# Kernel tuning notes

Hardware: AMD Instinct MI355X
Metric: run time of the kernel (lower is better)

The kernel has to match this reference:

```python
import jax, jax.numpy as jnp
import numpy as np

# ---- static config (from init_kwargs) ----
CANVAS = (4, 32, 32)        # (C1, C2, C3) latent video canvas
TILE = (4, 8, 8)            # (T1, T2, T3) tile dims
KERNEL = (1, 3, 3)          # sliding kernel in tile units
ROPE_DIMS = (16, 56, 56)    # per-axis RoPE dims, sums to head_dim
THETA = 256.0
HEADS = 16
HEAD_DIM = 128
HIDDEN = HEADS * HEAD_DIM
B = 1
L = CANVAS[0] * CANVAS[1] * CANVAS[2]
EPS = 1e-6
SCALE = HEAD_DIM ** -0.5
D = tuple(CANVAS[i] // TILE[i] for i in range(3))   # tile grid (D1,D2,D3)
N_TILES = D[0] * D[1] * D[2]
T_TOK = TILE[0] * TILE[1] * TILE[2]


def _rope_tables():
    # 3D meshgrid positions, per-axis 1D rotary tables concatenated on feature dim
    grids = np.meshgrid(*[np.arange(c, dtype=np.float32) for c in CANVAS], indexing='ij')
    cos_l, sin_l = [], []
    for i in range(3):
        dim = ROPE_DIMS[i]
        freqs = 1.0 / (THETA ** (np.arange(0, dim, 2, dtype=np.float32) / dim))
        ang = grids[i].reshape(-1)[:, None] * freqs[None, :]          # [L, dim/2]
        cos_l.append(np.repeat(np.cos(ang), 2, axis=1))               # [L, dim]
        sin_l.append(np.repeat(np.sin(ang), 2, axis=1))
    return jnp.asarray(np.concatenate(cos_l, 1)), jnp.asarray(np.concatenate(sin_l, 1))


def _window_indices():
    # For each query tile (d1,d2,d3): attends to a clamped kernel window of kv tiles
    d1, d2, d3 = np.meshgrid(*[np.arange(d) for d in D], indexing='ij')
    idx = []
    for i, dg in enumerate((d1, d2, d3)):
        k = KERNEL[i]
        s = np.clip(dg - k // 2, 0, D[i] - k)                         # window start, [D1,D2,D3]
        shape = [1, 1, 1]
        shape[i] = k
        idx.append(s[..., None, None, None] + np.arange(k).reshape(shape))
    flat = (idx[0] * D[1] + idx[1]) * D[2] + idx[2]                   # [D1,D2,D3,k1,k2,k3]
    kt = KERNEL[0] * KERNEL[1] * KERNEL[2]
    return jnp.asarray(flat.reshape(N_TILES, kt))


def _tile(x):
    # [B,H,L,E] -> [B,H,N_tiles,T_tok,E] with (D1,T1,D2,T2,D3,T3) -> (D1,D2,D3,T1,T2,T3)
    b, h, _, e = x.shape
    x = x.reshape(b, h, D[0], TILE[0], D[1], TILE[1], D[2], TILE[2], e)
    x = x.transpose(0, 1, 2, 4, 6, 3, 5, 7, 8)
    return x.reshape(b, h, N_TILES, T_TOK, e)


def _untile(x):
    # inverse of _tile: [B,H,N_tiles,T_tok,E] -> [B,H,L,E]
    b, h, _, _, e = x.shape
    x = x.reshape(b, h, D[0], D[1], D[2], TILE[0], TILE[1], TILE[2], e)
    x = x.transpose(0, 1, 2, 5, 3, 6, 4, 7, 8)
    return x.reshape(b, h, L, e)


def _rms(x, g):
    return x * jax.lax.rsqrt(jnp.mean(x * x, axis=-1, keepdims=True) + EPS) * g


def _rope(x, cos, sin):
    # x: [B,L,H,E], cos/sin: [L,E]; rotate-half in interleaved pairs
    xr = x.reshape(*x.shape[:-1], HEAD_DIM // 2, 2)
    rot = jnp.stack([-xr[..., 1], xr[..., 0]], axis=-1).reshape(x.shape)
    return x * cos[None, :, None, :] + rot * sin[None, :, None, :]


def _forward(hidden_states, Wq, bq, Wk, bk, Wv, bv, Wo, bo, gq, gk):
    cos, sin = _rope_tables()
    q = hidden_states @ Wq + bq
    k = hidden_states @ Wk + bk
    v = hidden_states @ Wv + bv
    q = q.reshape(B, L, HEADS, HEAD_DIM)
    k = k.reshape(B, L, HEADS, HEAD_DIM)
    v = v.reshape(B, L, HEADS, HEAD_DIM)
    q = _rope(_rms(q, gq), cos, sin)
    k = _rope(_rms(k, gk), cos, sin)
    q = q.transpose(0, 2, 1, 3)  # [B,H,L,E]
    k = k.transpose(0, 2, 1, 3)
    v = v.transpose(0, 2, 1, 3)
    qt = _tile(q)                # [B,H,N,T,E]
    kt = _tile(k)
    vt = _tile(v)
    win = _window_indices()      # [N, Kt]
    kt_w = kt[:, :, win].reshape(B, HEADS, N_TILES, -1, HEAD_DIM)  # [B,H,N,Kt*T,E]
    vt_w = vt[:, :, win].reshape(B, HEADS, N_TILES, -1, HEAD_DIM)
    s = jnp.einsum('bhnqe,bhnke->bhnqk', qt, kt_w) * SCALE
    p = jax.nn.softmax(s, axis=-1)
    o = jnp.einsum('bhnqk,bhnke->bhnqe', p, vt_w)
    o = _untile(o).transpose(0, 2, 1, 3).reshape(B, L, HIDDEN)
    return o @ Wo + bo


def setup_inputs() -> dict:
    key = jax.random.key(0)
    ks = jax.random.split(key, 6)
    w = 0.02
    return {
        'hidden_states': jax.random.normal(ks[0], (B, L, HIDDEN), jnp.float32),
        'Wq': jax.random.normal(ks[1], (HIDDEN, HIDDEN), jnp.float32) * w,
        'bq': jnp.zeros((HIDDEN,), jnp.float32),
        'Wk': jax.random.normal(ks[2], (HIDDEN, HIDDEN), jnp.float32) * w,
        'bk': jnp.zeros((HIDDEN,), jnp.float32),
        'Wv': jax.random.normal(ks[3], (HIDDEN, HIDDEN), jnp.float32) * w,
        'bv': jnp.zeros((HIDDEN,), jnp.float32),
        'Wo': jax.random.normal(ks[4], (HIDDEN, HIDDEN), jnp.float32) * w,
        'bo': jnp.zeros((HIDDEN,), jnp.float32),
        'gq': jnp.ones((HEAD_DIM,), jnp.float32),
        'gk': jnp.ones((HEAD_DIM,), jnp.float32),
    }


def reference(hidden_states, Wq, bq, Wk, bk, Wv, bv, Wo, bo, gq, gk):
    return _forward(hidden_states, Wq, bq, Wk, bk, Wv, bv, Wo, bo, gq, gk)
```

## Files before the change

### kernel.cpp

```cpp
#include <hip/hip_runtime.h>
#include <math.h>

typedef __attribute__((ext_vector_type(8))) short bf16x8;
typedef __attribute__((ext_vector_type(4))) float f32x4;
typedef unsigned short u16;
typedef unsigned int u32;

#define N_TOK 4096
#define HID   2048
#define N_HEAD 16
#define HDIM  128
#define QK_SCALE 0.08838834764831845f
#define LOG2E_   1.4426950408889634f

__device__ __forceinline__ u16 f2bf(float x) {
  union { float f; u32 u; } v; v.f = x;
  u32 r = v.u + 0x7fffu + ((v.u >> 16) & 1u);
  return (u16)(r >> 16);
}

__device__ __forceinline__ u32 cvtpk(float lo, float hi) {
  u32 r;
  asm("v_cvt_pk_bf16_f32 %0, %1, %2" : "=v"(r) : "v"(lo), "v"(hi));
  return r;
}

__device__ __forceinline__ void async16(const void* g, void* l) {
  __builtin_amdgcn_global_load_lds(
      (const __attribute__((address_space(1))) void*)g,
      (__attribute__((address_space(3))) void*)l, 16, 0, 0);
}

#define MFMA(a, b, c) __builtin_amdgcn_mfma_f32_16x16x32_bf16((a), (b), (c), 0, 0, 0)

__global__ void k_rope(float* __restrict__ cosT, float* __restrict__ sinT) {
  int l = blockIdx.x;
  int p = threadIdx.x;
  int c1 = l >> 10, c2 = (l >> 5) & 31, c3 = l & 31;
  int pos, j; float dim;
  if (p < 8)       { pos = c1; j = p;      dim = 16.f; }
  else if (p < 36) { pos = c2; j = p - 8;  dim = 56.f; }
  else             { pos = c3; j = p - 36; dim = 56.f; }
  float freq = exp2f(-8.0f * (2.0f * (float)j) / dim);
  float ang = (float)pos * freq;
  float s, c;
  sincosf(ang, &s, &c);
  cosT[l * 64 + p] = c;
  sinT[l * 64 + p] = s;
}

__global__ __launch_bounds__(256) void k_cvt_x(const float* __restrict__ X, u16* __restrict__ Xb) {
  int i = blockIdx.x * 256 + threadIdx.x;
  float4 v = ((const float4*)X)[i];
  ushort4 o;
  o.x = f2bf(v.x); o.y = f2bf(v.y); o.z = f2bf(v.z); o.w = f2bf(v.w);
  ((ushort4*)Xb)[i] = o;
}

__global__ __launch_bounds__(256) void k_tw(const float* __restrict__ Wq, const float* __restrict__ Wk,
                                            const float* __restrict__ Wv, const float* __restrict__ Wo,
                                            u16* __restrict__ WT) {
  int z = blockIdx.z;
  const float* W = (z == 0) ? Wq : (z == 1) ? Wk : (z == 2) ? Wv : Wo;
  u16* dst = WT + (size_t)z * 2048 * 2048;
  __shared__ __align__(16) float T[64][69];
  int n0 = blockIdx.x * 64, k0 = blockIdx.y * 64;
  int tid = threadIdx.x;
  int r = tid >> 4, c4 = tid & 15;
#pragma unroll
  for (int i = 0; i < 4; ++i) {
    int row = r + i * 16;
    float4 v = *(const float4*)(W + (size_t)(k0 + row) * 2048 + n0 + c4 * 4);
    T[row][c4 * 4 + 0] = v.x; T[row][c4 * 4 + 1] = v.y;
    T[row][c4 * 4 + 2] = v.z; T[row][c4 * 4 + 3] = v.w;
  }
  __syncthreads();
#pragma unroll
  for (int i = 0; i < 4; ++i) {
    int row = r + i * 16;
    ushort4 o;
    o.x = f2bf(T[c4 * 4 + 0][row]);
    o.y = f2bf(T[c4 * 4 + 1][row]);
    o.z = f2bf(T[c4 * 4 + 2][row]);
    o.w = f2bf(T[c4 * 4 + 3][row]);
    *(ushort4*)(dst + (size_t)(n0 + row) * 2048 + k0 + c4 * 4) = o;
  }
}


#define VM8 asm volatile("s_waitcnt vmcnt(8)" ::: "memory");
#define VM6 asm volatile("s_waitcnt vmcnt(6)" ::: "memory");
#define VMNONE

#define STAGEU(SB, SAB, SH, ST) do {                                            \
    int st_ = (ST) < Tk ? (ST) : Tk - 1;                                        \
    const char* src_ = ((SAB) ? Bp : Ap) + (size_t)((SH) * 128) * Kb + (size_t)st_ * 128; \
    char* dstl_ = &Lds[SB][SAB][SH][0];                                         \
    _Pragma("unroll")                                                           \
    for (int i_ = 0; i_ < 2; ++i_) {                                            \
      int flat_ = tid + 512 * i_;                                               \
      int row_ = flat_ >> 3, sb_ = flat_ & 7;                                   \
      async16(src_ + (size_t)row_ * Kb + ((sb_ ^ (row_ & 7)) << 4), dstl_ + flat_ * 16); \
    }                                                                           \
  } while (0)

#define PHASE(BUF, MH, NH, READA, VMOP, SB, SAB, SH, ST) do {                   \
    VMOP                                                                        \
    __builtin_amdgcn_s_barrier();                                               \
    asm volatile("" ::: "memory");                                              \
    bf16x8 bb[2][2];                                                            \
    const char* Lm = &Lds[BUF][0][MH][0];                                       \
    const char* Ln = &Lds[BUF][1][NH][0];                                       \
    if (READA) {                                                                \
      _Pragma("unroll")                                                         \
      for (int kk = 0; kk < 2; ++kk)                                            \
        _Pragma("unroll")                                                       \
        for (int mf = 0; mf < 4; ++mf) {                                        \
          int row = wmIdx * 64 + mf * 16 + cl;                                  \
          af[kk][mf] = *(const bf16x8*)(Lm + row * 128 + (((kk * 4 + g) ^ (row & 7)) << 4)); \
        }                                                                       \
    }                                                                           \
    _Pragma("unroll")                                                           \
    for (int kk = 0; kk < 2; ++kk)                                              \
      _Pragma("unroll")                                                         \
      for (int nf = 0; nf < 2; ++nf) {                                          \
        int row = wnIdx * 32 + nf * 16 + cl;                                    \
        bb[kk][nf] = *(const bf16x8*)(Ln + row * 128 + (((kk * 4 + g) ^ (row & 7)) << 4)); \
      }                                                                         \
    STAGEU(SB, SAB, SH, ST);                                                    \
    __builtin_amdgcn_s_setprio(1);                                              \
    _Pragma("unroll")                                                           \
    for (int kk = 0; kk < 2; ++kk)                                              \
      _Pragma("unroll")                                                         \
      for (int mf = 0; mf < 4; ++mf)                                            \
        _Pragma("unroll")                                                       \
        for (int nf = 0; nf < 2; ++nf)                                          \
          acc[(MH) * 4 + mf][(NH) * 2 + nf] =                                   \
              MFMA(af[kk][mf], bb[kk][nf], acc[(MH) * 4 + mf][(NH) * 2 + nf]);  \
    __builtin_amdgcn_s_setprio(0);                                              \
  } while (0)

__global__ __launch_bounds__(512, 2) void k_gemm8(const u16* __restrict__ A, const u16* __restrict__ Bt,
                                                  const float* __restrict__ b0, const float* __restrict__ b1,
                                                  const float* __restrict__ b2, float* __restrict__ C,
                                                  int gn, int K, int ldc) {
  __shared__ __align__(16) char Lds[2][2][2][16384];
  int tid = threadIdx.x;
  int lane = tid & 63, wid = tid >> 6;
  int g = lane >> 4, cl = lane & 15;
  int wmIdx = wid >> 2, wnIdx = wid & 3;
  int nwg = gridDim.x;
  int wg = (int)blockIdx.x;
  int cpx = nwg >> 3;
  wg = (wg & 7) * cpx + (wg >> 3);
  int bm = wg / gn, bn = wg % gn;
  size_t Kb = (size_t)K * 2;
  const char* Ap = (const char*)A + (size_t)bm * 256 * Kb;
  const char* Bp = (const char*)Bt + (size_t)bn * 256 * Kb;
  int Tk = K >> 6;

  f32x4 acc[8][4] = {};
  bf16x8 af[2][4];

  STAGEU(0, 0, 0, 0);
  STAGEU(0, 1, 0, 0);
  STAGEU(0, 0, 1, 0);
  STAGEU(0, 1, 1, 0);
  STAGEU(1, 0, 0, 1);
  STAGEU(1, 1, 0, 1);

  int nIter = Tk >> 1;
  for (int it = 0; it < nIter; ++it) {
    int t = 2 * it;
    PHASE(0, 0, 0, 1, VM8,    1, 0, 1, t + 1);
    PHASE(0, 0, 1, 0, VM6,    1, 1, 1, t + 1);
    PHASE(0, 1, 0, 1, VMNONE, 0, 0, 0, t + 2);
    PHASE(0, 1, 1, 0, VMNONE, 0, 1, 0, t + 2);
    PHASE(1, 0, 0, 1, VM8,    0, 0, 1, t + 2);
    PHASE(1, 0, 1, 0, VM6,    0, 1, 1, t + 2);
    PHASE(1, 1, 0, 1, VMNONE, 1, 0, 0, t + 3);
    PHASE(1, 1, 1, 0, VMNONE, 1, 1, 0, t + 3);
  }

#pragma unroll
  for (int mfp = 0; mfp < 8; ++mfp) {
    int rowBase = (mfp < 4 ? wmIdx * 64 + mfp * 16 : 128 + wmIdx * 64 + (mfp - 4) * 16) + g * 4;
    int rowG = bm * 256 + rowBase;
#pragma unroll
    for (int nfp = 0; nfp < 4; ++nfp) {
      int colLoc = (nfp < 2 ? wnIdx * 32 + nfp * 16 : 128 + wnIdx * 32 + (nfp - 2) * 16) + cl;
      int col = bn * 256 + colLoc;
      int z = col >> 11;
      const float* bp = (z == 0) ? b0 : (z == 1) ? b1 : b2;
      float bv = bp[col & 2047];
#pragma unroll
      for (int rr = 0; rr < 4; ++rr)
        C[(size_t)(rowG + rr) * ldc + col] = acc[mfp][nfp][rr] + bv;
    }
  }
}

__global__ __launch_bounds__(256) void k_prep_qk(const float* __restrict__ src, int stride,
                                                 const float* __restrict__ gg,
                                                 const float* __restrict__ cosT, const float* __restrict__ sinT,
                                                 u16* __restrict__ dst, int isk) {
  int job = blockIdx.x * 4 + (threadIdx.x >> 6);
  int lane = threadIdx.x & 63;
  int tok = job & 4095, h = job >> 12;
  const float* row = src + (size_t)tok * stride + h * 128;
  float2 x = *(const float2*)(row + lane * 2);
  float ss = x.x * x.x + x.y * x.y;
#pragma unroll
  for (int m = 1; m < 64; m <<= 1) ss += __shfl_xor(ss, m, 64);
  float rms = rsqrtf(ss * (1.0f / 128.0f) + 1e-6f);
  float x0 = x.x * rms * gg[lane * 2];
  float x1 = x.y * rms * gg[lane * 2 + 1];
  float c = cosT[tok * 64 + lane], s = sinT[tok * 64 + lane];
  float y0 = x0 * c - x1 * s;
  float y1 = x1 * c + x0 * s;
  if (!isk) { y0 *= QK_SCALE * LOG2E_; y1 *= QK_SCALE * LOG2E_; }
  u32 pk = cvtpk(y0, y1);
  int c1 = tok >> 10, c2 = (tok >> 5) & 31, c3 = tok & 31;
  int n = (c2 >> 3) * 4 + (c3 >> 3);
  int t = c1 * 64 + (c2 & 7) * 8 + (c3 & 7);
  size_t rowidx = (size_t)(h * 16 + n) * 256 + t;
  if (!isk) {
    ((u32*)dst)[rowidx * 64 + lane] = pk;
  } else {
    char* base = (char*)dst + rowidx * 256;
    *(u32*)(base + ((((lane >> 2) ^ (t & 7)) << 4) + (lane & 3) * 4)) = pk;
  }
}

__global__ __launch_bounds__(256) void k_prep_v(const float* __restrict__ src, int stride,
                                                u16* __restrict__ Vt) {
  __shared__ __align__(16) u16 T[128][72];
  int tid = threadIdx.x;
  int h = blockIdx.x >> 6, n = (blockIdx.x >> 2) & 15, ch = blockIdx.x & 3;
  int d2 = n >> 2, d3 = n & 3;
  int tc = tid >> 2, cq = tid & 3;
  int tok = (ch * 32 + d2 * 8 + (tc >> 3)) * 32 + d3 * 8 + (tc & 7);
  const float* sp = src + (size_t)tok * stride + h * 128;
#pragma unroll
  for (int i = 0; i < 8; ++i) {
    int d0 = cq * 4 + i * 16;
    float4 v = *(const float4*)(sp + d0);
    T[d0 + 0][tc] = f2bf(v.x); T[d0 + 1][tc] = f2bf(v.y);
    T[d0 + 2][tc] = f2bf(v.z); T[d0 + 3][tc] = f2bf(v.w);
  }
  __syncthreads();
  int d = tid >> 1, half = tid & 1;
  char* dstb = (char*)Vt + ((size_t)((h * 16 + n) * 4 + ch) * 128 + d) * 128;
#pragma unroll
  for (int b = 0; b < 4; ++b) {
    int blk = half * 4 + b;
    uint4 val = *(const uint4*)&T[d][blk * 8];
    *(uint4*)(dstb + ((blk ^ (d & 7)) << 4)) = val;
  }
}

__global__ __launch_bounds__(512) void k_attn(const u16* __restrict__ Qt, const u16* __restrict__ Kt,
                                              const u16* __restrict__ Vt, u16* __restrict__ AO) {
  __shared__ __align__(16) char Kl[2][16384];
  __shared__ __align__(16) char Vl[2][16384];
  __shared__ __align__(16) char Pl[8][4096];
  int tid = threadIdx.x;
  int lane = tid & 63, wid = tid >> 6;
  int g = lane >> 4, cl = lane & 15;
  int bid = (int)blockIdx.x;
  int xcd = bid & 7, i = bid >> 3;
  int h = xcd * 2 + (i >> 4);
  int n = i & 15;
  int d2 = n >> 2, d3 = n & 3;
  int s2 = d2 - 1; s2 = s2 < 0 ? 0 : (s2 > 1 ? 1 : s2);
  int s3 = d3 - 1; s3 = s3 < 0 ? 0 : (s3 > 1 ? 1 : s3);
  int q0 = wid * 32;

  bf16x8 qf[2][4];
  const char* Qb = (const char*)Qt + (size_t)(h * 16 + n) * 256 * 256;
#pragma unroll
  for (int nq = 0; nq < 2; ++nq)
#pragma unroll
    for (int kf = 0; kf < 4; ++kf)
      qf[nq][kf] = *(const bf16x8*)(Qb + (q0 + nq * 16 + cl) * 256 + kf * 64 + g * 16);

  f32x4 o[2][8] = {};
  float L0 = 0.f, L1 = 0.f;

  auto stage = [&](int buf, int c) {
    int kvi = c >> 2, cc = c & 3;
    int i2 = kvi / 3, i3 = kvi - i2 * 3;
    int kvt = (s2 + i2) * 4 + (s3 + i3);
    const char* Kb = (const char*)Kt + ((size_t)((h * 16 + kvt) * 256 + cc * 64)) * 256;
    const char* Vb = (const char*)Vt + ((size_t)((h * 16 + kvt) * 4 + cc)) * 16384;
#pragma unroll
    for (int i_ = 0; i_ < 2; ++i_) {
      int flat = tid + 512 * i_;
      async16(Kb + flat * 16, &Kl[buf][0] + flat * 16);
      async16(Vb + flat * 16, &Vl[buf][0] + flat * 16);
    }
  };

  stage(0, 0);
  __syncthreads();

  char* Pw = &Pl[wid][0];
  for (int c = 0; c < 36; ++c) {
    int cur = c & 1;
    if (c + 1 < 36) stage(cur ^ 1, c + 1);
    const char* Kc = &Kl[cur][0];
    f32x4 st[4][2] = {};
    __builtin_amdgcn_s_setprio(1);
#pragma unroll
    for (int ks = 0; ks < 4; ++ks) {
      bf16x8 af[4];
#pragma unroll
      for (int mk = 0; mk < 4; ++mk) {
        int row = mk * 16 + cl;
        af[mk] = *(const bf16x8*)(Kc + row * 256 + (((ks * 4 + g) ^ (row & 7)) << 4));
      }
#pragma unroll
      for (int mk = 0; mk < 4; ++mk) {
        st[mk][0] = MFMA(af[mk], qf[0][ks], st[mk][0]);
        st[mk][1] = MFMA(af[mk], qf[1][ks], st[mk][1]);
      }
    }
    __builtin_amdgcn_s_setprio(0);
#pragma unroll
    for (int mk = 0; mk < 4; ++mk)
#pragma unroll
      for (int r = 0; r < 4; ++r) {
        float p0 = exp2f(st[mk][0][r]);
        float p1 = exp2f(st[mk][1][r]);
        st[mk][0][r] = p0; L0 += p0;
        st[mk][1][r] = p1; L1 += p1;
      }
#pragma unroll
    for (int nq = 0; nq < 2; ++nq) {
      int q = nq * 16 + cl;
#pragma unroll
      for (int mk = 0; mk < 4; ++mk)
#pragma unroll
        for (int rp = 0; rp < 2; ++rp) {
          u32 pk = cvtpk(st[mk][nq][rp * 2], st[mk][nq][rp * 2 + 1]);
          int kv = mk * 16 + g * 4 + rp * 2;
          *(u32*)(Pw + q * 128 + (((kv >> 3) ^ (q & 7)) << 4) + (kv & 7) * 2) = pk;
        }
    }
    const char* Vc = &Vl[cur][0];
    __builtin_amdgcn_s_setprio(1);
#pragma unroll
    for (int ks = 0; ks < 2; ++ks) {
      bf16x8 pf0, pf1, vf[8];
      {
        int q = cl;
        pf0 = *(const bf16x8*)(Pw + q * 128 + (((ks * 4 + g) ^ (q & 7)) << 4));
        q = 16 + cl;
        pf1 = *(const bf16x8*)(Pw + q * 128 + (((ks * 4 + g) ^ (q & 7)) << 4));
      }
#pragma unroll
      for (int nd = 0; nd < 8; ++nd) {
        int d = nd * 16 + cl;
        vf[nd] = *(const bf16x8*)(Vc + d * 128 + (((ks * 4 + g) ^ (d & 7)) << 4));
      }
#pragma unroll
      for (int nd = 0; nd < 8; ++nd) {
        o[0][nd] = MFMA(pf0, vf[nd], o[0][nd]);
        o[1][nd] = MFMA(pf1, vf[nd], o[1][nd]);
      }
    }
    __builtin_amdgcn_s_setprio(0);
    __syncthreads();
  }
  L0 += __shfl_xor(L0, 16, 64); L0 += __shfl_xor(L0, 32, 64);
  L1 += __shfl_xor(L1, 16, 64); L1 += __shfl_xor(L1, 32, 64);
  float lr0[4], lr1[4];
#pragma unroll
  for (int r = 0; r < 4; ++r) {
    lr0[r] = 1.0f / __shfl(L0, g * 4 + r, 64);
    lr1[r] = 1.0f / __shfl(L1, g * 4 + r, 64);
  }
#pragma unroll
  for (int mo = 0; mo < 2; ++mo)
#pragma unroll
    for (int r = 0; r < 4; ++r) {
      int t = q0 + mo * 16 + g * 4 + r;
      int t1 = t >> 6, t2 = (t >> 3) & 7, t3 = t & 7;
      int tok = (t1 * 32 + d2 * 8 + t2) * 32 + d3 * 8 + t3;
      u16* orow = AO + (size_t)tok * HID + h * HDIM;
      float lr = (mo == 0) ? lr0[r] : lr1[r];
#pragma unroll
      for (int nd = 0; nd < 8; ++nd)
        orow[nd * 16 + cl] = f2bf(o[mo][nd][r] * lr);
    }
}

extern "C" void kernel_launch(void* const* d_in, const int* in_sizes, int n_in,
                              void* d_out, int out_size, void* d_ws, size_t ws_size,
                              hipStream_t stream) {
  const float* X  = (const float*)d_in[0];
  const float* Wq = (const float*)d_in[1];
  const float* bq = (const float*)d_in[2];
  const float* Wk = (const float*)d_in[3];
  const float* bk = (const float*)d_in[4];
  const float* Wv = (const float*)d_in[5];
  const float* bv = (const float*)d_in[6];
  const float* Wo = (const float*)d_in[7];
  const float* bo = (const float*)d_in[8];
  const float* gq = (const float*)d_in[9];
  const float* gk = (const float*)d_in[10];

  char* ws = (char*)d_ws;
  size_t off = 0;
  auto alloc = [&](size_t bytes) { void* p = ws + off; off = (off + bytes + 255) & ~(size_t)255; return p; };

  u16*   Xb  = (u16*)alloc((size_t)N_TOK * HID * 2);
  u16*   WT  = (u16*)alloc((size_t)4 * 2048 * 2048 * 2);
  float* COS = (float*)alloc((size_t)N_TOK * 64 * 4);
  float* SIN = (float*)alloc((size_t)N_TOK * 64 * 4);
  u16*   Qt  = (u16*)alloc((size_t)N_TOK * HID * 2);
  u16*   Kt  = (u16*)alloc((size_t)N_TOK * HID * 2);
  u16*   Vt  = (u16*)alloc((size_t)N_TOK * HID * 2);
  u16*   AO  = (u16*)alloc((size_t)N_TOK * HID * 2);
  size_t fixed = off;
  size_t needF = fixed + (size_t)N_TOK * 6144 * 4 + 256;
  bool fused = (ws_size >= needF);
  float* PF = (float*)alloc(fused ? (size_t)N_TOK * 6144 * 4 : (size_t)N_TOK * 2048 * 4);
  float* OUT = (float*)d_out;

  k_rope<<<N_TOK, 64, 0, stream>>>(COS, SIN);
  k_cvt_x<<<(N_TOK * HID / 4) / 256, 256, 0, stream>>>(X, Xb);
  k_tw<<<dim3(32, 32, 4), 256, 0, stream>>>(Wq, Wk, Wv, Wo, WT);

  if (fused) {
    k_gemm8<<<16 * 24, 512, 0, stream>>>(Xb, WT, bq, bk, bv, PF, 24, 2048, 6144);
    k_prep_qk<<<16384, 256, 0, stream>>>(PF + 0,    6144, gq, COS, SIN, Qt, 0);
    k_prep_qk<<<16384, 256, 0, stream>>>(PF + 2048, 6144, gk, COS, SIN, Kt, 1);
    k_prep_v <<<1024,  256, 0, stream>>>(PF + 4096, 6144, Vt);
  } else {
    k_gemm8<<<16 * 8, 512, 0, stream>>>(Xb, WT + (size_t)0 * 2048 * 2048, bq, bq, bq, PF, 8, 2048, 2048);
    k_prep_qk<<<16384, 256, 0, stream>>>(PF, 2048, gq, COS, SIN, Qt, 0);
    k_gemm8<<<16 * 8, 512, 0, stream>>>(Xb, WT + (size_t)1 * 2048 * 2048, bk, bk, bk, PF, 8, 2048, 2048);
    k_prep_qk<<<16384, 256, 0, stream>>>(PF, 2048, gk, COS, SIN, Kt, 1);
    k_gemm8<<<16 * 8, 512, 0, stream>>>(Xb, WT + (size_t)2 * 2048 * 2048, bv, bv, bv, PF, 8, 2048, 2048);
    k_prep_v<<<1024, 256, 0, stream>>>(PF, 2048, Vt);
  }

  k_attn<<<256, 512, 0, stream>>>(Qt, Kt, Vt, AO);

  k_gemm8<<<16 * 8, 512, 0, stream>>>(AO, WT + (size_t)3 * 2048 * 2048, bo, bo, bo, OUT, 8, 2048, 2048);
}
```

Baseline: 460.8 us.

## Restructure GEMM main loop into reordered quadrant pipeline with XCD-aware tile mapping

Rewrites the 256x256 bf16 GEMM main loop from eight fixed phases per two k-steps into four MFMA quadrants per k-step. B fragments are kept in two register sets and reused across quadrants in the order (0,0),(0,1),(1,1),(1,0), and LDS reads, async global stages and barriers are interleaved around them. It also replaces the generic XCD swizzle with a fixed mapping that groups M and N tiles per XCD for L2 reuse. The extra barriers, and the mapping's assumption about the grid shape (bm spanning 16 row tiles, gn divisible by 4), add sync cost and could give wrong tile coverage for other shapes.

```diff
diff --git a/kernel.cpp b/kernel.cpp
--- a/kernel.cpp
+++ b/kernel.cpp
@@ -88,9 +88,7 @@
 }
 
 
-#define VM8 asm volatile("s_waitcnt vmcnt(8)" ::: "memory");
 #define VM6 asm volatile("s_waitcnt vmcnt(6)" ::: "memory");
-#define VMNONE
 
 #define STAGEU(SB, SAB, SH, ST) do {                                            \
     int st_ = (ST) < Tk ? (ST) : Tk - 1;                                        \
@@ -104,30 +102,31 @@
     }                                                                           \
   } while (0)
 
-#define PHASE(BUF, MH, NH, READA, VMOP, SB, SAB, SH, ST) do {                   \
-    VMOP                                                                        \
-    __builtin_amdgcn_s_barrier();                                               \
-    asm volatile("" ::: "memory");                                              \
-    bf16x8 bb[2][2];                                                            \
-    const char* Lm = &Lds[BUF][0][MH][0];                                       \
-    const char* Ln = &Lds[BUF][1][NH][0];                                       \
-    if (READA) {                                                                \
+#define RD_A(HALF) do {                                                         \
+    const char* Lm_ = &Lds[buf][0][HALF][0];                                    \
+    _Pragma("unroll")                                                           \
+    for (int kk = 0; kk < 2; ++kk)                                              \
       _Pragma("unroll")                                                         \
-      for (int kk = 0; kk < 2; ++kk)                                            \
-        _Pragma("unroll")                                                       \
-        for (int mf = 0; mf < 4; ++mf) {                                        \
-          int row = wmIdx * 64 + mf * 16 + cl;                                  \
-          af[kk][mf] = *(const bf16x8*)(Lm + row * 128 + (((kk * 4 + g) ^ (row & 7)) << 4)); \
-        }                                                                       \
-    }                                                                           \
+      for (int mf = 0; mf < 4; ++mf) {                                          \
+        int row = wmIdx * 64 + mf * 16 + cl;                                    \
+        af[kk][mf] = *(const bf16x8*)(Lm_ + row * 128 + (((kk * 4 + g) ^ (row & 7)) << 4)); \
+      }                                                                         \
+  } while (0)
+
+#define RD_B(DST, HALF) do {                                                    \
+    const char* Ln_ = &Lds[buf][1][HALF][0];                                    \
     _Pragma("unroll")                                                           \
     for (int kk = 0; kk < 2; ++kk)                                              \
       _Pragma("unroll")                                                         \
       for (int nf = 0; nf < 2; ++nf) {                                          \
         int row = wnIdx * 32 + nf * 16 + cl;                                    \
-        bb[kk][nf] = *(const bf16x8*)(Ln + row * 128 + (((kk * 4 + g) ^ (row & 7)) << 4)); \
+        DST[kk][nf] = *(const bf16x8*)(Ln_ + row * 128 + (((kk * 4 + g) ^ (row & 7)) << 4)); \
       }                                                                         \
-    STAGEU(SB, SAB, SH, ST);                                                    \
+  } while (0)
+
+#define DO_MFMA(MH, NH, FB) do {                                                \
+    __builtin_amdgcn_s_barrier();                                               \
+    asm volatile("s_waitcnt lgkmcnt(0)" ::: "memory");                          \
     __builtin_amdgcn_s_setprio(1);                                              \
     _Pragma("unroll")                                                           \
     for (int kk = 0; kk < 2; ++kk)                                              \
@@ -136,50 +135,58 @@
         _Pragma("unroll")                                                       \
         for (int nf = 0; nf < 2; ++nf)                                          \
           acc[(MH) * 4 + mf][(NH) * 2 + nf] =                                   \
-              MFMA(af[kk][mf], bb[kk][nf], acc[(MH) * 4 + mf][(NH) * 2 + nf]);  \
+              MFMA(af[kk][mf], FB[kk][nf], acc[(MH) * 4 + mf][(NH) * 2 + nf]);  \
     __builtin_amdgcn_s_setprio(0);                                              \
+    __builtin_amdgcn_s_barrier();                                               \
   } while (0)
 
 __global__ __launch_bounds__(512, 2) void k_gemm8(const u16* __restrict__ A, const u16* __restrict__ Bt,
-                                                  const float* __restrict__ b0, const float* __restrict__ b1,
-                                                  const float* __restrict__ b2, float* __restrict__ C,
+                                                  const float* __restrict__ bz0, const float* __restrict__ bz1,
+                                                  const float* __restrict__ bz2, float* __restrict__ C,
                                                   int gn, int K, int ldc) {
   __shared__ __align__(16) char Lds[2][2][2][16384];
   int tid = threadIdx.x;
   int lane = tid & 63, wid = tid >> 6;
   int g = lane >> 4, cl = lane & 15;
   int wmIdx = wid >> 2, wnIdx = wid & 3;
-  int nwg = gridDim.x;
-  int wg = (int)blockIdx.x;
-  int cpx = nwg >> 3;
-  wg = (wg & 7) * cpx + (wg >> 3);
-  int bm = wg / gn, bn = wg % gn;
+  int bid = (int)blockIdx.x;
+  int xcd = bid & 7, l = bid >> 3;
+  int sliceW = gn >> 2;
+  int bm = (xcd & 1) * 8 + (l & 7);
+  int bn = (xcd >> 1) * sliceW + (l >> 3);
   size_t Kb = (size_t)K * 2;
   const char* Ap = (const char*)A + (size_t)bm * 256 * Kb;
   const char* Bp = (const char*)Bt + (size_t)bn * 256 * Kb;
   int Tk = K >> 6;
 
   f32x4 acc[8][4] = {};
-  bf16x8 af[2][4];
+  bf16x8 af[2][4], fb0[2][2], fb1[2][2];
 
   STAGEU(0, 0, 0, 0);
   STAGEU(0, 1, 0, 0);
+  STAGEU(0, 1, 1, 0);
   STAGEU(0, 0, 1, 0);
-  STAGEU(0, 1, 1, 0);
   STAGEU(1, 0, 0, 1);
   STAGEU(1, 1, 0, 1);
-
-  int nIter = Tk >> 1;
-  for (int it = 0; it < nIter; ++it) {
-    int t = 2 * it;
-    PHASE(0, 0, 0, 1, VM8,    1, 0, 1, t + 1);
-    PHASE(0, 0, 1, 0, VM6,    1, 1, 1, t + 1);
-    PHASE(0, 1, 0, 1, VMNONE, 0, 0, 0, t + 2);
-    PHASE(0, 1, 1, 0, VMNONE, 0, 1, 0, t + 2);
-    PHASE(1, 0, 0, 1, VM8,    0, 0, 1, t + 2);
-    PHASE(1, 0, 1, 0, VM6,    0, 1, 1, t + 2);
-    PHASE(1, 1, 0, 1, VMNONE, 1, 0, 0, t + 3);
-    PHASE(1, 1, 1, 0, VMNONE, 1, 1, 0, t + 3);
+  STAGEU(1, 1, 1, 1);
+  VM6
+  __builtin_amdgcn_s_barrier();
+
+  for (int t = 0; t < Tk; ++t) {
+    int buf = t & 1, obuf = buf ^ 1;
+    RD_A(0);
+    RD_B(fb0, 0);
+    STAGEU(obuf, 0, 1, t + 1);
+    DO_MFMA(0, 0, fb0);
+    RD_B(fb1, 1);
+    STAGEU(buf, 0, 0, t + 2);
+    DO_MFMA(0, 1, fb1);
+    RD_A(1);
+    STAGEU(buf, 1, 0, t + 2);
+    DO_MFMA(1, 1, fb1);
+    STAGEU(buf, 1, 1, t + 2);
+    VM6
+    DO_MFMA(1, 0, fb0);
   }
 
 #pragma unroll
@@ -191,7 +198,7 @@
       int colLoc = (nfp < 2 ? wnIdx * 32 + nfp * 16 : 128 + wnIdx * 32 + (nfp - 2) * 16) + cl;
       int col = bn * 256 + colLoc;
       int z = col >> 11;
-      const float* bp = (z == 0) ? b0 : (z == 1) ? b1 : b2;
+      const float* bp = (z == 0) ? bz0 : (z == 1) ? bz1 : bz2;
       float bv = bp[col & 2047];
 #pragma unroll
       for (int rr = 0; rr < 4; ++rr)
```

Result: no change. 467.3 us (+1.4%).
